# Optimization experiments

Hardware: AMD Instinct MI355X
Metric: run time of the kernel (lower is better)

Reference implementation:

```python
import jax, jax.numpy as jnp
import numpy as np

N_NODES = 100000
N_EDGES = 1600000
D_IN = 128
D_HID = 128
LATENT = 64
N_GRAPHS = 512


def setup_inputs() -> dict:
    key = jax.random.key(0)
    ks = jax.random.split(key, 10)
    x = jax.random.normal(ks[0], (N_NODES, D_IN), dtype=jnp.float32)
    edge_index = jax.random.randint(ks[1], (2, N_EDGES), 0, N_NODES, dtype=jnp.int64)
    batch = jnp.sort(jax.random.randint(ks[2], (N_NODES,), 0, N_GRAPHS, dtype=jnp.int64))
    def lin(k, fan_in, fan_out):
        return jax.random.normal(k, (fan_in, fan_out), dtype=jnp.float32) / np.sqrt(fan_in)
    W1 = lin(ks[3], D_IN, D_HID); b1 = jnp.zeros((D_HID,), jnp.float32)
    W2 = lin(ks[4], D_HID, D_HID); b2 = jnp.zeros((D_HID,), jnp.float32)
    W3 = lin(ks[5], D_HID, 2 * LATENT); b3 = jnp.zeros((2 * LATENT,), jnp.float32)
    return {"x": x, "edge_index": edge_index, "batch": batch,
            "W1": W1, "b1": b1, "W2": W2, "b2": b2, "W3": W3, "b3": b3}


def _gcn_norm(edge_index, n_nodes):
    # PyG GCNConv default: add self-loops, symmetric normalization
    loop = jnp.arange(n_nodes, dtype=edge_index.dtype)
    src = jnp.concatenate([edge_index[0], loop])
    dst = jnp.concatenate([edge_index[1], loop])
    deg = jax.ops.segment_sum(jnp.ones_like(dst, dtype=jnp.float32), dst,
                              num_segments=n_nodes)
    dinv = jnp.where(deg > 0, jax.lax.rsqrt(deg), 0.0)
    norm = dinv[src] * dinv[dst]  # [E + N]
    return src, dst, norm


def _gcn_conv(x, W, b, src, dst, norm, n_nodes):
    h = x @ W                               # [N, d_out]
    msg = h[src] * norm[:, None]            # gather + scale, [E+N, d_out]
    agg = jax.ops.segment_sum(msg, dst, num_segments=n_nodes)
    return agg + b


def reference(x, edge_index, batch, W1, b1, W2, b2, W3, b3):
    n = x.shape[0]
    src, dst, norm = _gcn_norm(edge_index, n)
    h = jax.nn.relu(_gcn_conv(x, W1, b1, src, dst, norm, n))
    h = jax.nn.relu(_gcn_conv(h, W2, b2, src, dst, norm, n))
    h = _gcn_conv(h, W3, b3, src, dst, norm, n)
    # scatter_mean over batch ids -> [num_graphs, 2*latent]
    cnt = jax.ops.segment_sum(jnp.ones((n,), jnp.float32), batch,
                              num_segments=N_GRAPHS)
    summed = jax.ops.segment_sum(h, batch, num_segments=N_GRAPHS)
    return summed / jnp.maximum(cnt, 1.0)[:, None]
```

## Files before the change

### kernel.cpp

```cpp
#include <hip/hip_runtime.h>
#include <stdint.h>

typedef unsigned short u16;
typedef unsigned int   u32;

#define N_NODES  100000
#define N_EDGES  1600000
#define DFEAT    128
#define N_GRAPHS 512

#define NBKT   391
#define EPB    8192
#define NBLK_E 196
#define LBUF   8192
#define GB     782

typedef float f32x4 __attribute__((ext_vector_type(4)));
typedef short s16x8 __attribute__((ext_vector_type(8)));

__device__ __forceinline__ float bflo(u32 u) { return __uint_as_float(u << 16); }
__device__ __forceinline__ float bfhi(u32 u) { return __uint_as_float(u & 0xffff0000u); }
__device__ __forceinline__ u16 f2bf(float f) {
  u32 u = __float_as_uint(f);
  return (u16)((u + 0x7fffu + ((u >> 16) & 1u)) >> 16);
}
__device__ __forceinline__ u32 pack2(float f0, float f1) {
  return (u32)f2bf(f0) | ((u32)f2bf(f1) << 16);
}

__device__ __forceinline__ int ld_src(const int* ei, int m, int e) {
  return m ? ei[2 * e] : ei[e];
}
__device__ __forceinline__ int ld_dst(const int* ei, int m, int e) {
  return m ? ei[2 * (N_EDGES + e)] : ei[N_EDGES + e];
}

__device__ __forceinline__ int detect_m_block(const int* __restrict__ ei, int* sm) {
  int t = threadIdx.x;
  if (t < 64) {
    int v = ei[2 * t + 1];
    unsigned long long b = __ballot(v != 0);
    if (t == 0) *sm = (b == 0ull) ? 1 : 0;
  }
  __syncthreads();
  return *sm;
}

#define LP 136

__global__ __launch_bounds__(256) void mega_k(const float* __restrict__ x,
                                              const int* __restrict__ ei,
                                              int* __restrict__ ghist,
                                              const float* __restrict__ W1,
                                              const float* __restrict__ W2,
                                              const float* __restrict__ W3,
                                              u16* __restrict__ T2, u16* __restrict__ T3,
                                              int* __restrict__ flag,
                                              u16* __restrict__ Y) {
  __shared__ u16 sX[128 * LP];
  __shared__ u16 sW[128 * LP];
  __shared__ int hist[NBKT];
  __shared__ int sm;
  int tid = threadIdx.x, b = blockIdx.x;

  if (b < GB) {
    int r0 = b * 128;
    for (int c = tid; c < 2048; c += 256) {
      int n = c & 127, k0 = (c >> 7) * 8;
#pragma unroll
      for (int j = 0; j < 8; j++)
        sW[n * LP + k0 + j] = f2bf(W1[(size_t)(k0 + j) * DFEAT + n]);
    }
    for (int c = tid; c < 2048; c += 256) {
      int row = c >> 4, off = (c & 15) * 8;
      int grow = r0 + row;
      uint4 o = make_uint4(0, 0, 0, 0);
      if (grow < N_NODES) {
        const float* px = x + (size_t)grow * DFEAT + off;
        float4 v0 = *(const float4*)px;
        float4 v1 = *(const float4*)(px + 4);
        o.x = pack2(v0.x, v0.y); o.y = pack2(v0.z, v0.w);
        o.z = pack2(v1.x, v1.y); o.w = pack2(v1.z, v1.w);
      }
      *(uint4*)(&sX[row * LP + off]) = o;
    }
    __syncthreads();

    int wave = tid >> 6, lane = tid & 63;
    int q = lane >> 4, r = lane & 15;
    int wr0 = wave * 32;

    f32x4 acc[2][8];
#pragma unroll
    for (int m = 0; m < 2; m++)
#pragma unroll
      for (int i = 0; i < 8; i++) acc[m][i] = (f32x4){0.f, 0.f, 0.f, 0.f};

#pragma unroll
    for (int kk = 0; kk < 4; kk++) {
      int k0 = kk * 32;
      s16x8 a0 = *(const s16x8*)(&sX[(wr0 + r) * LP + k0 + q * 8]);
      s16x8 a1 = *(const s16x8*)(&sX[(wr0 + 16 + r) * LP + k0 + q * 8]);
#pragma unroll
      for (int nt = 0; nt < 8; nt++) {
        s16x8 bb = *(const s16x8*)(&sW[(nt * 16 + r) * LP + k0 + q * 8]);
        acc[0][nt] = __builtin_amdgcn_mfma_f32_16x16x32_bf16(a0, bb, acc[0][nt], 0, 0, 0);
        acc[1][nt] = __builtin_amdgcn_mfma_f32_16x16x32_bf16(a1, bb, acc[1][nt], 0, 0, 0);
      }
    }

#pragma unroll
    for (int m = 0; m < 2; m++) {
#pragma unroll
      for (int i = 0; i < 4; i++) {
        int grow = r0 + wr0 + m * 16 + q * 4 + i;
        if (grow < N_NODES) {
#pragma unroll
          for (int nt = 0; nt < 8; nt++)
            Y[(size_t)grow * DFEAT + nt * 16 + r] = f2bf(acc[m][nt][i]);
        }
      }
    }
    return;
  }

  if (b < GB + NBLK_E) {
    int hb = b - GB;
    int m = detect_m_block(ei, &sm);
    for (int i = tid; i < NBKT; i += 256) hist[i] = 0;
    __syncthreads();
    int e0 = hb * EPB;
#pragma unroll
    for (int p = 0; p < EPB / 256; p++) {
      int e = e0 + p * 256 + tid;
      if (e < N_EDGES) atomicAdd(&hist[ld_dst(ei, m, e) >> 8], 1);
    }
    __syncthreads();
    for (int i = tid; i < NBKT; i += 256) ghist[hb * NBKT + i] = hist[i];
    return;
  }

  int r = b - GB - NBLK_E;
  if (r < 2) {
    const float* W = (r == 0) ? W2 : W3;
    u16* T         = (r == 0) ? T2 : T3;
    for (int i = tid; i < DFEAT * DFEAT; i += 256) {
      int n = i >> 7, k = i & 127;
      T[i] = f2bf(W[k * DFEAT + n]);
    }
  } else {
    if (tid < 64) {
      int v = ei[2 * tid + 1];
      unsigned long long mm = __ballot(v != 0);
      if (tid == 0) *flag = (mm == 0ull) ? 1 : 0;
    }
  }
}

__device__ __forceinline__ void scan_lds391(const int* arr, int* bb, int* sc) {
  int t = threadIdx.x;
  int v0 = arr[t];
  sc[t] = v0;
  for (int off = 1; off < 256; off <<= 1) {
    __syncthreads(); int add = (t >= off) ? sc[t - off] : 0;
    __syncthreads(); sc[t] += add;
  }
  __syncthreads();
  bb[t] = sc[t] - v0;
  int base256 = sc[255];
  __syncthreads();
  int v1 = (t < NBKT - 256) ? arr[256 + t] : 0;
  sc[t] = v1;
  for (int off = 1; off < 256; off <<= 1) {
    __syncthreads(); int add = (t >= off) ? sc[t - off] : 0;
    __syncthreads(); sc[t] += add;
  }
  __syncthreads();
  if (t < NBKT - 256) bb[256 + t] = base256 + sc[t] - v1;
  if (t == 0) bb[NBKT] = N_EDGES;
  __syncthreads();
}

__global__ __launch_bounds__(256) void scatterC_k(const int* __restrict__ ei,
                                                  const int* __restrict__ ghist,
                                                  u32* __restrict__ colpk) {
  __shared__ int sm;
  __shared__ int colsum[NBKT];
  __shared__ int colpre[NBKT];
  __shared__ int cur[NBKT];
  __shared__ int bb[NBKT + 1];
  __shared__ int sc[256];
  int t = threadIdx.x, b = blockIdx.x;
  int m = detect_m_block(ei, &sm);
  for (int k = t; k < NBKT; k += 256) {
    int tot = 0, pre = 0;
    for (int b2 = 0; b2 < NBLK_E; b2++) {
      int v = ghist[b2 * NBKT + k];
      tot += v;
      pre += (b2 < b) ? v : 0;
    }
    colsum[k] = tot; colpre[k] = pre;
  }
  __syncthreads();
  scan_lds391(colsum, bb, sc);
  for (int k = t; k < NBKT; k += 256) cur[k] = bb[k] + colpre[k];
  __syncthreads();
  int e0 = b * EPB;
#pragma unroll
  for (int p = 0; p < EPB / 256; p++) {
    int e = e0 + p * 256 + t;
    if (e < N_EDGES) {
      int d = ld_dst(ei, m, e);
      int s = ld_src(ei, m, e);
      int pos = atomicAdd(&cur[d >> 8], 1);
      colpk[pos] = (u32)s | ((u32)(d & 255) << 24);
    }
  }
}

__global__ __launch_bounds__(256) void fillD_k(const int* __restrict__ ghist,
                                               const u32* __restrict__ colpk,
                                               int* __restrict__ colarr,
                                               int* __restrict__ rowptr,
                                               float* __restrict__ dinv) {
  __shared__ int hist[256];
  __shared__ int cur[256];
  __shared__ int lbuf[LBUF];
  __shared__ int colsum[NBKT];
  __shared__ int bb[NBKT + 1];
  __shared__ int sc[256];
  int t = threadIdx.x, b = blockIdx.x;
  for (int k = t; k < NBKT; k += 256) {
    int tot = 0;
    for (int b2 = 0; b2 < NBLK_E; b2++) tot += ghist[b2 * NBKT + k];
    colsum[k] = tot;
  }
  __syncthreads();
  scan_lds391(colsum, bb, sc);
  int base = bb[b], end = bb[b + 1], cnt = end - base;
  hist[t] = 0;
  __syncthreads();
  for (int i = t; i < cnt; i += 256) atomicAdd(&hist[colpk[base + i] >> 24], 1);
  __syncthreads();
  int c = hist[t];
  cur[t] = c;
  for (int off = 1; off < 256; off <<= 1) {
    __syncthreads(); int add = (t >= off) ? cur[t - off] : 0;
    __syncthreads(); cur[t] += add;
  }
  __syncthreads();
  int excl = cur[t] - c;
  int node = b * 256 + t;
  if (node < N_NODES) {
    rowptr[node] = base + excl;
    dinv[node] = rsqrtf((float)(c + 1));
  }
  if (b == NBKT - 1 && t == 0) rowptr[N_NODES] = N_EDGES;
  __syncthreads();
  cur[t] = excl;
  __syncthreads();
  for (int i = t; i < cnt; i += 256) {
    u32 v = colpk[base + i];
    int slot = atomicAdd(&cur[v >> 24], 1);
    if (slot < LBUF) lbuf[slot] = (int)(v & 0x00FFFFFFu);
  }
  __syncthreads();
  for (int i = t; i < cnt; i += 256) colarr[base + i] = lbuf[i];
}

struct Acc8 {
  float a0, a1, a2, a3, a4, a5, a6, a7;
  __device__ __forceinline__ void zero() {
    a0 = a1 = a2 = a3 = a4 = a5 = a6 = a7 = 0.f;
  }
  __device__ __forceinline__ void addv(uint4 v) {
    a0 += bflo(v.x); a1 += bfhi(v.x); a2 += bflo(v.y); a3 += bfhi(v.y);
    a4 += bflo(v.z); a5 += bfhi(v.z); a6 += bflo(v.w); a7 += bfhi(v.w);
  }
  __device__ __forceinline__ void fmav(uint4 v, float s) {
    a0 = fmaf(bflo(v.x), s, a0); a1 = fmaf(bfhi(v.x), s, a1);
    a2 = fmaf(bflo(v.y), s, a2); a3 = fmaf(bfhi(v.y), s, a3);
    a4 = fmaf(bflo(v.z), s, a4); a5 = fmaf(bfhi(v.z), s, a5);
    a6 = fmaf(bflo(v.w), s, a6); a7 = fmaf(bfhi(v.w), s, a7);
  }
};

__device__ __forceinline__ Acc8 gather_plain(const u32* __restrict__ HS,
                                             int s, int e, int node, int fp,
                                             const int* __restrict__ colidx) {
  Acc8 A; A.zero();
  A.addv(*(const uint4*)(HS + (size_t)node * 64 + fp * 4));
  int j = s;
  for (; j + 4 <= e; j += 4) {
    int i0 = colidx[j], i1 = colidx[j + 1], i2 = colidx[j + 2], i3 = colidx[j + 3];
    uint4 w0 = *(const uint4*)(HS + (size_t)i0 * 64 + fp * 4);
    uint4 w1 = *(const uint4*)(HS + (size_t)i1 * 64 + fp * 4);
    uint4 w2 = *(const uint4*)(HS + (size_t)i2 * 64 + fp * 4);
    uint4 w3 = *(const uint4*)(HS + (size_t)i3 * 64 + fp * 4);
    A.addv(w0); A.addv(w1); A.addv(w2); A.addv(w3);
  }
  for (; j < e; j++) {
    A.addv(*(const uint4*)(HS + (size_t)colidx[j] * 64 + fp * 4));
  }
  return A;
}

__device__ __forceinline__ Acc8 gather_scaled(const u32* __restrict__ HS,
                                              const float* __restrict__ dinv,
                                              int s, int e, int node, int fp,
                                              const int* __restrict__ colidx) {
  Acc8 A; A.zero();
  A.fmav(*(const uint4*)(HS + (size_t)node * 64 + fp * 4), dinv[node]);
  int j = s;
  for (; j + 4 <= e; j += 4) {
    int i0 = colidx[j], i1 = colidx[j + 1], i2 = colidx[j + 2], i3 = colidx[j + 3];
    float s0 = dinv[i0], s1 = dinv[i1], s2 = dinv[i2], s3 = dinv[i3];
    uint4 w0 = *(const uint4*)(HS + (size_t)i0 * 64 + fp * 4);
    uint4 w1 = *(const uint4*)(HS + (size_t)i1 * 64 + fp * 4);
    uint4 w2 = *(const uint4*)(HS + (size_t)i2 * 64 + fp * 4);
    uint4 w3 = *(const uint4*)(HS + (size_t)i3 * 64 + fp * 4);
    A.fmav(w0, s0); A.fmav(w1, s1); A.fmav(w2, s2); A.fmav(w3, s3);
  }
  for (; j < e; j++) {
    int i0 = colidx[j];
    A.fmav(*(const uint4*)(HS + (size_t)i0 * 64 + fp * 4), dinv[i0]);
  }
  return A;
}

__global__ __launch_bounds__(256) void aggmm_k(const u32* __restrict__ HS,
                                               const float* __restrict__ dinv,
                                               const int* __restrict__ rowptr,
                                               const int* __restrict__ colidx,
                                               const float* __restrict__ bias,
                                               const u16* __restrict__ Wt,
                                               u16* __restrict__ Y,
                                               int src_scaled) {
  __shared__ u16 sX[16 * LP];
  int t = threadIdx.x;
  int r0b = blockIdx.x * 16;
  int lrow = t >> 4, fp = t & 15;
  int node = r0b + lrow;
  int s = rowptr[node], e = rowptr[node + 1];

  Acc8 A;
  if (src_scaled) A = gather_plain(HS, s, e, node, fp, colidx);
  else            A = gather_scaled(HS, dinv, s, e, node, fp, colidx);

  float dv = dinv[node];
  float4 b0 = *(const float4*)(bias + fp * 8);
  float4 b1 = *(const float4*)(bias + fp * 8 + 4);
  float r0f = fmaxf(A.a0 * dv + b0.x, 0.f), r1f = fmaxf(A.a1 * dv + b0.y, 0.f);
  float r2f = fmaxf(A.a2 * dv + b0.z, 0.f), r3f = fmaxf(A.a3 * dv + b0.w, 0.f);
  float r4f = fmaxf(A.a4 * dv + b1.x, 0.f), r5f = fmaxf(A.a5 * dv + b1.y, 0.f);
  float r6f = fmaxf(A.a6 * dv + b1.z, 0.f), r7f = fmaxf(A.a7 * dv + b1.w, 0.f);
  uint4 o;
  o.x = pack2(r0f, r1f); o.y = pack2(r2f, r3f);
  o.z = pack2(r4f, r5f); o.w = pack2(r6f, r7f);
  *(uint4*)(&sX[lrow * LP + fp * 8]) = o;
  __syncthreads();

  int wave = t >> 6, lane = t & 63;
  int q = lane >> 4, r = lane & 15;
  int nt0 = wave * 2, nt1 = wave * 2 + 1;

  f32x4 acc0 = (f32x4){0.f, 0.f, 0.f, 0.f};
  f32x4 acc1 = (f32x4){0.f, 0.f, 0.f, 0.f};
#pragma unroll
  for (int kk = 0; kk < 4; kk++) {
    int k0 = kk * 32;
    s16x8 a  = *(const s16x8*)(&sX[r * LP + k0 + q * 8]);
    s16x8 w0 = *(const s16x8*)(Wt + (size_t)(nt0 * 16 + r) * DFEAT + k0 + q * 8);
    s16x8 w1 = *(const s16x8*)(Wt + (size_t)(nt1 * 16 + r) * DFEAT + k0 + q * 8);
    acc0 = __builtin_amdgcn_mfma_f32_16x16x32_bf16(a, w0, acc0, 0, 0, 0);
    acc1 = __builtin_amdgcn_mfma_f32_16x16x32_bf16(a, w1, acc1, 0, 0, 0);
  }
#pragma unroll
  for (int i = 0; i < 4; i++) {
    int grow = r0b + q * 4 + i;
    float dvv = dinv[grow];
    Y[(size_t)grow * DFEAT + nt0 * 16 + r] = f2bf(acc0[i] * dvv);
    Y[(size_t)grow * DFEAT + nt1 * 16 + r] = f2bf(acc1[i] * dvv);
  }
}

__global__ __launch_bounds__(256) void agg_k(const u32* __restrict__ HS,
                                             const float* __restrict__ dinv,
                                             const int* __restrict__ rowptr,
                                             const int* __restrict__ colidx,
                                             const float* __restrict__ bias,
                                             u32* __restrict__ OUT) {
  int t = threadIdx.x;
  int node = blockIdx.x * 16 + (t >> 4);
  int fp = t & 15;
  int s = rowptr[node], e = rowptr[node + 1];

  Acc8 A = gather_plain(HS, s, e, node, fp, colidx);

  float dv = dinv[node];
  float4 b0 = *(const float4*)(bias + fp * 8);
  float4 b1 = *(const float4*)(bias + fp * 8 + 4);
  uint4 o;
  o.x = pack2(A.a0 * dv + b0.x, A.a1 * dv + b0.y);
  o.y = pack2(A.a2 * dv + b0.z, A.a3 * dv + b0.w);
  o.z = pack2(A.a4 * dv + b1.x, A.a5 * dv + b1.y);
  o.w = pack2(A.a6 * dv + b1.z, A.a7 * dv + b1.w);
  *(uint4*)(OUT + (size_t)node * 64 + fp * 4) = o;
}

__device__ __forceinline__ int lower_bound_i(const int* a, int n, int key, int shift) {
  int lo = 0, hi = n;
  while (lo < hi) {
    int mid = (lo + hi) >> 1;
    if (a[mid << shift] < key) lo = mid + 1; else hi = mid;
  }
  return lo;
}

__global__ __launch_bounds__(256) void pool_k(const u32* __restrict__ H,
                                              const int* __restrict__ batch,
                                              const int* __restrict__ flag,
                                              float* __restrict__ OUT) {
  int g = blockIdx.x;
  int m = *flag;
  int lo = lower_bound_i(batch, N_NODES, g, m);
  int hi = lower_bound_i(batch, N_NODES, g + 1, m);
  int cnt = hi - lo;
  int d2 = threadIdx.x & 63;
  int half = threadIdx.x >> 6;
  float a0 = 0.f, a1 = 0.f;
  for (int row = lo + half; row < hi; row += 4) {
    u32 v = H[(size_t)row * 64 + d2];
    a0 += bflo(v); a1 += bfhi(v);
  }
  __shared__ float red0[256], red1[256];
  red0[threadIdx.x] = a0; red1[threadIdx.x] = a1;
  __syncthreads();
  if (threadIdx.x < 64) {
    float s0 = red0[d2] + red0[d2 + 64] + red0[d2 + 128] + red0[d2 + 192];
    float s1 = red1[d2] + red1[d2 + 64] + red1[d2 + 128] + red1[d2 + 192];
    float inv = 1.0f / fmaxf((float)cnt, 1.0f);
    OUT[g * DFEAT + 2 * d2]     = s0 * inv;
    OUT[g * DFEAT + 2 * d2 + 1] = s1 * inv;
  }
}


extern "C" void kernel_launch(void* const* d_in, const int* in_sizes, int n_in,
                              void* d_out, int out_size, void* d_ws, size_t ws_size,
                              hipStream_t stream) {
  const float* x   = (const float*)d_in[0];
  const int* ei    = (const int*)d_in[1];
  const int* batch = (const int*)d_in[2];
  const float* W1  = (const float*)d_in[3];
  const float* b1  = (const float*)d_in[4];
  const float* W2  = (const float*)d_in[5];
  const float* b2  = (const float*)d_in[6];
  const float* W3  = (const float*)d_in[7];
  const float* b3  = (const float*)d_in[8];
  float* out = (float*)d_out;

  char* p = (char*)d_ws;
  size_t off = 0;
  auto carve = [&](size_t bytes) -> void* {
    void* q = p + off;
    off = (off + bytes + 255) & ~(size_t)255;
    return q;
  };
  int*   flag   = (int*)carve(256);
  int*   ghist  = (int*)carve((size_t)NBLK_E * NBKT * 4);
  int*   rowptr = (int*)carve((N_NODES + 1) * 4);
  float* dinv   = (float*)carve(N_NODES * 4);
  u32*   colpk  = (u32*)carve((size_t)N_EDGES * 4);
  int*   colarr = (int*)carve((size_t)N_EDGES * 4);
  u16*   Wt2    = (u16*)carve(DFEAT * DFEAT * 2);
  u16*   Wt3    = (u16*)carve(DFEAT * DFEAT * 2);
  u32*   bufA   = (u32*)carve((size_t)N_NODES * 64 * 4);
  u32*   bufB   = (u32*)carve((size_t)N_NODES * 64 * 4);
  (void)ws_size;

  const int AB = N_NODES / 16;

  mega_k<<<GB + NBLK_E + 3, 256, 0, stream>>>(x, ei, ghist, W1, W2, W3, Wt2, Wt3,
                                              flag, (u16*)bufA);
  scatterC_k<<<NBLK_E, 256, 0, stream>>>(ei, ghist, colpk);
  fillD_k<<<NBKT, 256, 0, stream>>>(ghist, colpk, colarr, rowptr, dinv);
  aggmm_k<<<AB, 256, 0, stream>>>(bufA, dinv, rowptr, colarr, b1, Wt2, (u16*)bufB, 0);
  aggmm_k<<<AB, 256, 0, stream>>>(bufB, dinv, rowptr, colarr, b2, Wt3, (u16*)bufA, 1);
  agg_k<<<AB, 256, 0, stream>>>(bufA, dinv, rowptr, colarr, b3, bufB);
  pool_k<<<N_GRAPHS, 256, 0, stream>>>(bufB, batch, flag, out);
}
```

Measured before the change: 436.9 us.

## Halve GEMM row tile, alias LDS, and transpose ghist layout

The first-layer GEMM tile drops from 128 to 64 rows per block, which doubles the grid to 1563 blocks. The hist buffer now aliases the sX/sW LDS region, cutting LDS per block so more blocks can be resident. The per-block bucket histogram is stored bucket-major, so each thread's prefix and column-sum loops in scatterC_k and fillD_k read contiguous memory instead of striding by NBKT. In exchange, W1 is converted and loaded into LDS twice as often across the grid.

Result: faster. 418.9 us (-4.1%).

```diff
diff --git a/kernel.cpp b/kernel.cpp
--- a/kernel.cpp
+++ b/kernel.cpp
@@ -13,7 +13,7 @@
 #define EPB    8192
 #define NBLK_E 196
 #define LBUF   8192
-#define GB     782
+#define GB1    1563
 
 typedef float f32x4 __attribute__((ext_vector_type(4)));
 typedef short s16x8 __attribute__((ext_vector_type(8)));
@@ -57,21 +57,22 @@
                                               u16* __restrict__ T2, u16* __restrict__ T3,
                                               int* __restrict__ flag,
                                               u16* __restrict__ Y) {
-  __shared__ u16 sX[128 * LP];
-  __shared__ u16 sW[128 * LP];
-  __shared__ int hist[NBKT];
+  __shared__ char smem[(64 + 128) * LP * 2];
+  u16* sX = (u16*)smem;
+  u16* sW = (u16*)(smem + 64 * LP * 2);
+  int* hist = (int*)smem;
   __shared__ int sm;
   int tid = threadIdx.x, b = blockIdx.x;
 
-  if (b < GB) {
-    int r0 = b * 128;
+  if (b < GB1) {
+    int r0 = b * 64;
     for (int c = tid; c < 2048; c += 256) {
       int n = c & 127, k0 = (c >> 7) * 8;
 #pragma unroll
       for (int j = 0; j < 8; j++)
         sW[n * LP + k0 + j] = f2bf(W1[(size_t)(k0 + j) * DFEAT + n]);
     }
-    for (int c = tid; c < 2048; c += 256) {
+    for (int c = tid; c < 1024; c += 256) {
       int row = c >> 4, off = (c & 15) * 8;
       int grow = r0 + row;
       uint4 o = make_uint4(0, 0, 0, 0);
@@ -88,44 +89,37 @@
 
     int wave = tid >> 6, lane = tid & 63;
     int q = lane >> 4, r = lane & 15;
-    int wr0 = wave * 32;
-
-    f32x4 acc[2][8];
-#pragma unroll
-    for (int m = 0; m < 2; m++)
-#pragma unroll
-      for (int i = 0; i < 8; i++) acc[m][i] = (f32x4){0.f, 0.f, 0.f, 0.f};
+    int wr0 = wave * 16;
+
+    f32x4 acc[8];
+#pragma unroll
+    for (int i = 0; i < 8; i++) acc[i] = (f32x4){0.f, 0.f, 0.f, 0.f};
 
 #pragma unroll
     for (int kk = 0; kk < 4; kk++) {
       int k0 = kk * 32;
-      s16x8 a0 = *(const s16x8*)(&sX[(wr0 + r) * LP + k0 + q * 8]);
-      s16x8 a1 = *(const s16x8*)(&sX[(wr0 + 16 + r) * LP + k0 + q * 8]);
+      s16x8 a = *(const s16x8*)(&sX[(wr0 + r) * LP + k0 + q * 8]);
 #pragma unroll
       for (int nt = 0; nt < 8; nt++) {
         s16x8 bb = *(const s16x8*)(&sW[(nt * 16 + r) * LP + k0 + q * 8]);
-        acc[0][nt] = __builtin_amdgcn_mfma_f32_16x16x32_bf16(a0, bb, acc[0][nt], 0, 0, 0);
-        acc[1][nt] = __builtin_amdgcn_mfma_f32_16x16x32_bf16(a1, bb, acc[1][nt], 0, 0, 0);
+        acc[nt] = __builtin_amdgcn_mfma_f32_16x16x32_bf16(a, bb, acc[nt], 0, 0, 0);
       }
     }
 
 #pragma unroll
-    for (int m = 0; m < 2; m++) {
-#pragma unroll
-      for (int i = 0; i < 4; i++) {
-        int grow = r0 + wr0 + m * 16 + q * 4 + i;
-        if (grow < N_NODES) {
-#pragma unroll
-          for (int nt = 0; nt < 8; nt++)
-            Y[(size_t)grow * DFEAT + nt * 16 + r] = f2bf(acc[m][nt][i]);
-        }
+    for (int i = 0; i < 4; i++) {
+      int grow = r0 + wr0 + q * 4 + i;
+      if (grow < N_NODES) {
+#pragma unroll
+        for (int nt = 0; nt < 8; nt++)
+          Y[(size_t)grow * DFEAT + nt * 16 + r] = f2bf(acc[nt][i]);
       }
     }
     return;
   }
 
-  if (b < GB + NBLK_E) {
-    int hb = b - GB;
+  if (b < GB1 + NBLK_E) {
+    int hb = b - GB1;
     int m = detect_m_block(ei, &sm);
     for (int i = tid; i < NBKT; i += 256) hist[i] = 0;
     __syncthreads();
@@ -136,11 +130,11 @@
       if (e < N_EDGES) atomicAdd(&hist[ld_dst(ei, m, e) >> 8], 1);
     }
     __syncthreads();
-    for (int i = tid; i < NBKT; i += 256) ghist[hb * NBKT + i] = hist[i];
+    for (int i = tid; i < NBKT; i += 256) ghist[(size_t)i * NBLK_E + hb] = hist[i];
     return;
   }
 
-  int r = b - GB - NBLK_E;
+  int r = b - GB1 - NBLK_E;
   if (r < 2) {
     const float* W = (r == 0) ? W2 : W3;
     u16* T         = (r == 0) ? T2 : T3;
@@ -193,9 +187,10 @@
   int t = threadIdx.x, b = blockIdx.x;
   int m = detect_m_block(ei, &sm);
   for (int k = t; k < NBKT; k += 256) {
+    const int* row = ghist + (size_t)k * NBLK_E;
     int tot = 0, pre = 0;
     for (int b2 = 0; b2 < NBLK_E; b2++) {
-      int v = ghist[b2 * NBKT + k];
+      int v = row[b2];
       tot += v;
       pre += (b2 < b) ? v : 0;
     }
@@ -231,8 +226,9 @@
   __shared__ int sc[256];
   int t = threadIdx.x, b = blockIdx.x;
   for (int k = t; k < NBKT; k += 256) {
+    const int* row = ghist + (size_t)k * NBLK_E;
     int tot = 0;
-    for (int b2 = 0; b2 < NBLK_E; b2++) tot += ghist[b2 * NBKT + k];
+    for (int b2 = 0; b2 < NBLK_E; b2++) tot += row[b2];
     colsum[k] = tot;
   }
   __syncthreads();
@@ -468,7 +464,7 @@
     return q;
   };
   int*   flag   = (int*)carve(256);
-  int*   ghist  = (int*)carve((size_t)NBLK_E * NBKT * 4);
+  int*   ghist  = (int*)carve((size_t)NBKT * NBLK_E * 4);
   int*   rowptr = (int*)carve((N_NODES + 1) * 4);
   float* dinv   = (float*)carve(N_NODES * 4);
   u32*   colpk  = (u32*)carve((size_t)N_EDGES * 4);
@@ -481,8 +477,8 @@
 
   const int AB = N_NODES / 16;
 
-  mega_k<<<GB + NBLK_E + 3, 256, 0, stream>>>(x, ei, ghist, W1, W2, W3, Wt2, Wt3,
-                                              flag, (u16*)bufA);
+  mega_k<<<GB1 + NBLK_E + 3, 256, 0, stream>>>(x, ei, ghist, W1, W2, W3, Wt2, Wt3,
+                                               flag, (u16*)bufA);
   scatterC_k<<<NBLK_E, 256, 0, stream>>>(ei, ghist, colpk);
   fillD_k<<<NBKT, 256, 0, stream>>>(ghist, colpk, colarr, rowptr, dinv);
   aggmm_k<<<AB, 256, 0, stream>>>(bufA, dinv, rowptr, colarr, b1, Wt2, (u16*)bufB, 0);
```
